# Kernel optimization log

Hardware: AMD Instinct MI355X
Metric: run time of the kernel (lower is better)

Reference implementation:

```python
import jax, jax.numpy as jnp
import numpy as np

B, N, D, H = 8, 8192, 512, 8  # batch, seq, hidden, heads
DH = D // H


def _rope_tables(n, d, dtype=jnp.float32):
    # standard rotate-half RoPE tables over the full hidden dim (d/2 freq pairs)
    half = d // 2
    inv_freq = 1.0 / (10000.0 ** (np.arange(0, half, dtype=np.float32) / half))
    pos = np.arange(n, dtype=np.float32)
    ang = np.einsum('n,f->nf', pos, inv_freq)          # [N, D/2]
    ang = np.concatenate([ang, ang], axis=-1)          # [N, D]
    return jnp.asarray(np.cos(ang), dtype), jnp.asarray(np.sin(ang), dtype)


def setup_inputs() -> dict:
    key = jax.random.key(0)
    k1, k2 = jax.random.split(key)
    hidden_states = jax.random.normal(k1, (B, N, D), dtype=jnp.float32)
    num_layers = 24
    std = 0.02 / np.sqrt(2.0 * num_layers * D)
    W = jax.random.normal(k2, (D, D), dtype=jnp.float32) * std
    cos, sin = _rope_tables(N, D)
    return {"hidden_states": hidden_states, "W": W, "cos": cos, "sin": sin}


def _rotate_half(x):
    x1, x2 = jnp.split(x, 2, axis=-1)
    return jnp.concatenate([-x2, x1], axis=-1)


def reference(hidden_states, W, cos, sin):
    # dropout(p=0) in eval mode -> identity
    x = hidden_states * cos + _rotate_half(hidden_states) * sin  # RoPE, [B,N,D]
    q = jnp.einsum('bnd,ed->bne', x, W)                          # F.linear(x, W)
    qh = q.reshape(B, N, H, DH)
    xh = x.reshape(B, N, H, DH)
    # linear-complexity path: (K^T V) then Q @ (.), per head
    kv = jnp.einsum('bnhd,bnhe->bhde', xh, xh)   # [B,H,DH,DH]
    out = jnp.einsum('bnhd,bhde->bnhe', qh, kv)  # [B,N,H,DH]
    return out.reshape(B, N, D)
```

## Files before the change

### kernel.cpp

```cpp
#include <hip/hip_runtime.h>
#include <hip/hip_bf16.h>
#include <stdint.h>

#define BB 8
#define NN 8192
#define DD 512
#define HH 8
#define DHD 64
#define NCH 32

typedef __attribute__((ext_vector_type(8))) short bf16x8;
typedef __attribute__((ext_vector_type(4))) float f32x4;
typedef __attribute__((ext_vector_type(4))) float f4v;

__device__ __forceinline__ unsigned short f2bf(float f) {
  union { float f; unsigned int u; } v; v.f = f;
  return (unsigned short)((v.u + 0x7FFFu + ((v.u >> 16) & 1u)) >> 16);
}

__device__ __forceinline__ unsigned cvtpk(float lo, float hi) {
  unsigned r;
  asm("v_cvt_pk_bf16_f32 %0, %1, %2" : "=v"(r) : "v"(lo), "v"(hi));
  return r;
}

__device__ __forceinline__ void async16(const void* g, void* l) {
  __builtin_amdgcn_global_load_lds(
      (const __attribute__((address_space(1))) void*)g,
      (__attribute__((address_space(3))) void*)l, 16, 0, 0);
}

__global__ __launch_bounds__(1024, 4) void ropekv_kernel(
    const float* __restrict__ h, const float* __restrict__ cs,
    const float* __restrict__ sn, unsigned short* __restrict__ x,
    float* __restrict__ kvp, int nbh) {
  __shared__ __align__(16) unsigned int xt32[2][512 * 34];
  int blk = blockIdx.x;
  int chunk = blk & 31, b = blk >> 5;
  int tid = threadIdx.x;
  int wave = tid >> 6, lane = tid & 63;
  int rpar = lane & 1;
  int g = lane >> 1;
  int cf = g * 8;
  int l15 = lane & 15, q = lane >> 4;
  int head = wave >> 1;
  int half = wave & 1;
  int hd = head * 64;
  size_t row0 = (size_t)b * NN + (size_t)chunk * 256;
  int n0 = chunk * 256;

  f32x4 acc[2][4];
#pragma unroll
  for (int i = 0; i < 2; ++i)
#pragma unroll
    for (int j = 0; j < 4; ++j) acc[i][j] = (f32x4){0.f, 0.f, 0.f, 0.f};

  f4v ha[2][2], hb[2][2];

  auto loadt = [&](int t) {
#pragma unroll
    for (int p = 0; p < 2; ++p) {
      int r = 2 * (wave + 16 * p) + rpar;
      const float* hp = h + (row0 + t * 64 + r) * DD + cf;
      ha[p][0] = __builtin_nontemporal_load((const f4v*)hp);
      ha[p][1] = __builtin_nontemporal_load((const f4v*)(hp + 4));
      hb[p][0] = __builtin_nontemporal_load((const f4v*)(hp + 256));
      hb[p][1] = __builtin_nontemporal_load((const f4v*)(hp + 260));
    }
  };

  auto ropet = [&](int t) {
    int pb = t & 1;
#pragma unroll
    for (int p = 0; p < 2; ++p) {
      int r = 2 * (wave + 16 * p) + rpar;
      int nr = n0 + t * 64 + r;
      const float* cp = cs + (size_t)nr * DD + cf;
      const float* sp = sn + (size_t)nr * DD + cf;
      f4v c0 = *(const f4v*)cp, c1 = *(const f4v*)(cp + 4);
      f4v s0 = *(const f4v*)sp, s1 = *(const f4v*)(sp + 4);
      f4v xl0 = ha[p][0] * c0 - hb[p][0] * s0;
      f4v xl1 = ha[p][1] * c1 - hb[p][1] * s1;
      f4v xh0 = hb[p][0] * c0 + ha[p][0] * s0;
      f4v xh1 = hb[p][1] * c1 + ha[p][1] * s1;
      unsigned ml[4], mh[4];
      ml[0] = cvtpk(xl0.x, xl0.y);
      ml[1] = cvtpk(xl0.z, xl0.w);
      ml[2] = cvtpk(xl1.x, xl1.y);
      ml[3] = cvtpk(xl1.z, xl1.w);
      mh[0] = cvtpk(xh0.x, xh0.y);
      mh[1] = cvtpk(xh0.z, xh0.w);
      mh[2] = cvtpk(xh1.x, xh1.y);
      mh[3] = cvtpk(xh1.z, xh1.w);
      unsigned short* xp = x + (row0 + t * 64 + r) * DD + cf;
      uint4 st0; st0.x = ml[0]; st0.y = ml[1]; st0.z = ml[2]; st0.w = ml[3];
      uint4 st1; st1.x = mh[0]; st1.y = mh[1]; st1.z = mh[2]; st1.w = mh[3];
      *(uint4*)xp         = st0;
      *(uint4*)(xp + 256) = st1;
      unsigned pk[8];
#pragma unroll
      for (int k = 0; k < 4; ++k) {
        unsigned mine = rpar ? mh[k] : ml[k];
        unsigned send = rpar ? ml[k] : mh[k];
        unsigned recv = (unsigned)__shfl_xor((int)send, 1, 64);
        if (!rpar) {
          pk[2 * k]     = (mine & 0xffffu) | (recv << 16);
          pk[2 * k + 1] = (mine >> 16) | (recv & 0xffff0000u);
        } else {
          pk[2 * k]     = (recv & 0xffffu) | (mine << 16);
          pk[2 * k + 1] = (recv >> 16) | (mine & 0xffff0000u);
        }
      }
      int np = wave + 16 * p;
      int dbase = cf + (rpar ? 256 : 0);
      int rot = (g >> 1) & 7;
#pragma unroll
      for (int w = 0; w < 8; ++w) {
        int jj = (w + rot) & 7;
        xt32[pb][(dbase + jj) * 34 + np] = pk[jj];
      }
    }
  };

  auto mfmat = [&](int t) {
    const unsigned short* xt16 = (const unsigned short*)xt32[t & 1];
#pragma unroll
    for (int ks = 0; ks < 64; ks += 32) {
      bf16x8 af[2], bf[4];
#pragma unroll
      for (int i = 0; i < 2; ++i)
        af[i] = *(const bf16x8*)&xt16[(hd + half * 32 + i * 16 + l15) * 68 + ks + q * 8];
#pragma unroll
      for (int j = 0; j < 4; ++j)
        bf[j] = *(const bf16x8*)&xt16[(hd + j * 16 + l15) * 68 + ks + q * 8];
#pragma unroll
      for (int i = 0; i < 2; ++i)
#pragma unroll
        for (int j = 0; j < 4; ++j)
          acc[i][j] = __builtin_amdgcn_mfma_f32_16x16x32_bf16(af[i], bf[j], acc[i][j], 0, 0, 0);
    }
  };

  loadt(0);
  ropet(0);
  loadt(1);
  __syncthreads();
#pragma unroll
  for (int t = 0; t < 4; ++t) {
    if (t < 3) ropet(t + 1);
    if (t < 2) loadt(t + 2);
    mfmat(t);
    __syncthreads();
  }

  int bh = b * 8 + head;
  float* dst = kvp + ((size_t)chunk * nbh + bh) * 4096;
#pragma unroll
  for (int i = 0; i < 2; ++i)
#pragma unroll
    for (int j = 0; j < 4; ++j)
#pragma unroll
      for (int reg = 0; reg < 4; ++reg)
        dst[(half * 32 + i * 16 + q * 4 + reg) * 64 + j * 16 + l15] = acc[i][j][reg];
}

__global__ __launch_bounds__(512, 2) void wkvt_kernel(
    const float* __restrict__ W, const float* __restrict__ kvp,
    unsigned short* __restrict__ wkvt, int nbh) {
  __shared__ float kvs[64 * 16];
  __shared__ __align__(16) float ws[64 * 512];
  int blk = blockIdx.x;
  int bh = blk >> 2, eq = blk & 3;
  int b = bh >> 3, hh = bh & 7;
  int tid = threadIdx.x;
  if (tid < 256) {
    int idx = tid * 4;
    int d = idx >> 4, ec = idx & 15;
    f4v s = (f4v){0.f, 0.f, 0.f, 0.f};
    for (int c = 0; c < NCH; ++c)
      s += *(const f4v*)&kvp[((size_t)c * nbh + bh) * 4096 + d * 64 + eq * 16 + ec];
    *(f4v*)&kvs[idx] = s;
  }
#pragma unroll
  for (int i = 0; i < 16; ++i) {
    int idx = i * 2048 + tid * 4;
    *(f4v*)&ws[idx] = *(const f4v*)&W[(size_t)(hh * DHD + (idx >> 9)) * DD + (idx & 511)];
  }
  __syncthreads();
  int el = tid & 15, fg = tid >> 4;
  f4v av[4];
#pragma unroll
  for (int k = 0; k < 4; ++k) av[k] = (f4v){0.f, 0.f, 0.f, 0.f};
#pragma unroll 8
  for (int d = 0; d < 64; ++d) {
    float kvv = kvs[d * 16 + el];
    const f4v* wr = (const f4v*)&ws[d * DD + fg * 16];
#pragma unroll
    for (int k = 0; k < 4; ++k) av[k] += wr[k] * kvv;
  }
  unsigned short tb[16];
#pragma unroll
  for (int k = 0; k < 4; ++k) {
    tb[k * 4 + 0] = f2bf(av[k].x); tb[k * 4 + 1] = f2bf(av[k].y);
    tb[k * 4 + 2] = f2bf(av[k].z); tb[k * 4 + 3] = f2bf(av[k].w);
  }
  size_t ob = ((size_t)b * DD + hh * DHD + eq * 16 + el) * DD + fg * 16;
  *(uint4*)&wkvt[ob]     = *(uint4*)&tb[0];
  *(uint4*)&wkvt[ob + 8] = *(uint4*)&tb[8];
}

__global__ __launch_bounds__(256, 3) void gemm_kernel(const unsigned short* __restrict__ x,
                                                      const unsigned short* __restrict__ wkvt,
                                                      float* __restrict__ out) {
  __shared__ __align__(16) unsigned short As[128 * 64];
  __shared__ __align__(16) unsigned short Bs[128 * 64];
  int mt = blockIdx.x, ct = blockIdx.y, bz = blockIdx.z;
  int tid = threadIdx.x, wave = tid >> 6, lane = tid & 63;
  int wm = wave & 1, wn = wave >> 1;
  int l15 = lane & 15, q = lane >> 4;
  int lrow = lane >> 3, lcol = (lane & 7) * 8;
  const unsigned short* Ag = x    + ((size_t)bz * NN + mt * 128) * DD;
  const unsigned short* Bg = wkvt + ((size_t)bz * DD + ct * 128) * DD;
  f32x4 acc[4][4];
#pragma unroll
  for (int i = 0; i < 4; ++i)
#pragma unroll
    for (int j = 0; j < 4; ++j) acc[i][j] = (f32x4){0.f, 0.f, 0.f, 0.f};

  for (int kk = 0; kk < 512; kk += 64) {
#pragma unroll
    for (int i = 0; i < 4; ++i)
      async16(Ag + (size_t)(wave * 32 + i * 8 + lrow) * DD + kk + lcol,
              &As[(wave * 32 + i * 8) * 64]);
#pragma unroll
    for (int i = 0; i < 4; ++i)
      async16(Bg + (size_t)(wave * 32 + i * 8 + lrow) * DD + kk + lcol,
              &Bs[(wave * 32 + i * 8) * 64]);
    __syncthreads();
#pragma unroll
    for (int ks = 0; ks < 64; ks += 32) {
      bf16x8 a[4], bb[4];
#pragma unroll
      for (int i = 0; i < 4; ++i)
        a[i] = *(const bf16x8*)&As[(wm * 64 + i * 16 + l15) * 64 + ks + q * 8];
#pragma unroll
      for (int j = 0; j < 4; ++j)
        bb[j] = *(const bf16x8*)&Bs[(wn * 64 + j * 16 + l15) * 64 + ks + q * 8];
#pragma unroll
      for (int i = 0; i < 4; ++i)
#pragma unroll
        for (int j = 0; j < 4; ++j)
          acc[i][j] = __builtin_amdgcn_mfma_f32_16x16x32_bf16(a[i], bb[j], acc[i][j], 0, 0, 0);
    }
    __syncthreads();
  }
  float* ob = out + ((size_t)bz * NN + mt * 128 + wm * 64) * DD + ct * 128 + wn * 64;
#pragma unroll
  for (int i = 0; i < 4; ++i)
#pragma unroll
    for (int j = 0; j < 4; ++j) {
      int row = i * 16 + q * 4;
      int col = j * 16 + l15;
#pragma unroll
      for (int reg = 0; reg < 4; ++reg)
        __builtin_nontemporal_store(acc[i][j][reg], &ob[(size_t)(row + reg) * DD + col]);
    }
}

extern "C" void kernel_launch(void* const* d_in, const int* in_sizes, int n_in,
                              void* d_out, int out_size, void* d_ws, size_t ws_size,
                              hipStream_t stream) {
  (void)in_sizes; (void)n_in; (void)out_size;
  const float* h  = (const float*)d_in[0];
  const float* W  = (const float*)d_in[1];
  const float* cs = (const float*)d_in[2];
  const float* sn = (const float*)d_in[3];
  float* out = (float*)d_out;

  const size_t x_full     = (size_t)BB * NN * DD * 2;
  const size_t kvp_full   = (size_t)NCH * BB * HH * DHD * DHD * 4;
  const size_t wkvt_full  = (size_t)BB * DD * DD * 2;
  const size_t x_batch    = (size_t)NN * DD * 2;
  const size_t kvp_batch  = (size_t)NCH * HH * DHD * DHD * 4;
  const size_t wkvt_batch = (size_t)DD * DD * 2;

  if (ws_size >= x_full + kvp_full + wkvt_full) {
    unsigned short* xw   = (unsigned short*)d_ws;
    float*          kvp  = (float*)((char*)d_ws + x_full);
    unsigned short* wkvt = (unsigned short*)((char*)d_ws + x_full + kvp_full);
    ropekv_kernel<<<dim3(BB * 32), dim3(1024), 0, stream>>>(h, cs, sn, xw, kvp, BB * HH);
    wkvt_kernel<<<dim3(BB * HH * 4), dim3(512), 0, stream>>>(W, kvp, wkvt, BB * HH);
    gemm_kernel<<<dim3(NN / 128, DD / 128, BB), dim3(256), 0, stream>>>(xw, wkvt, out);
  } else {
    unsigned short* xw   = (unsigned short*)d_ws;
    float*          kvp  = (float*)((char*)d_ws + x_batch);
    unsigned short* wkvt = (unsigned short*)((char*)d_ws + x_batch + kvp_batch);
    for (int b = 0; b < BB; ++b) {
      ropekv_kernel<<<dim3(32), dim3(1024), 0, stream>>>(
          h + (size_t)b * NN * DD, cs, sn, xw, kvp, HH);
      wkvt_kernel<<<dim3(HH * 4), dim3(512), 0, stream>>>(W, kvp, wkvt, HH);
      gemm_kernel<<<dim3(NN / 128, DD / 128, 1), dim3(256), 0, stream>>>(
          xw, wkvt, out + (size_t)b * NN * DD);
    }
  }
}
```

Before: 322.1 us.

## Switch GEMM to 32x32x16 MFMA with XOR-swizzled LDS tiles

Rewrites the main GEMM inner loop to use 32x32x16 bf16 MFMA instructions in a 2x2 accumulator grid instead of the 4x4 grid of 16x16x32. The LDS tiles are loaded with an XOR swizzle on the 16-byte chunk index to avoid bank conflicts on the fragment reads. Launch bounds are raised to 4 blocks per CU. The larger MFMA needs fewer LDS fragment reads per FLOP. The risks are register pressure under the tighter occupancy bound and a strided output store pattern.

```diff
diff --git a/kernel.cpp b/kernel.cpp
--- a/kernel.cpp
+++ b/kernel.cpp
@@ -11,6 +11,7 @@
 
 typedef __attribute__((ext_vector_type(8))) short bf16x8;
 typedef __attribute__((ext_vector_type(4))) float f32x4;
+typedef __attribute__((ext_vector_type(16))) float f32x16;
 typedef __attribute__((ext_vector_type(4))) float f4v;
 
 __device__ __forceinline__ unsigned short f2bf(float f) {
@@ -209,7 +210,7 @@
   *(uint4*)&wkvt[ob + 8] = *(uint4*)&tb[8];
 }
 
-__global__ __launch_bounds__(256, 3) void gemm_kernel(const unsigned short* __restrict__ x,
+__global__ __launch_bounds__(256, 4) void gemm_kernel(const unsigned short* __restrict__ x,
                                                       const unsigned short* __restrict__ wkvt,
                                                       float* __restrict__ out) {
   __shared__ __align__(16) unsigned short As[128 * 64];
@@ -217,54 +218,68 @@
   int mt = blockIdx.x, ct = blockIdx.y, bz = blockIdx.z;
   int tid = threadIdx.x, wave = tid >> 6, lane = tid & 63;
   int wm = wave & 1, wn = wave >> 1;
-  int l15 = lane & 15, q = lane >> 4;
-  int lrow = lane >> 3, lcol = (lane & 7) * 8;
+  int l31 = lane & 31, hk = lane >> 5;
   const unsigned short* Ag = x    + ((size_t)bz * NN + mt * 128) * DD;
   const unsigned short* Bg = wkvt + ((size_t)bz * DD + ct * 128) * DD;
-  f32x4 acc[4][4];
-#pragma unroll
-  for (int i = 0; i < 4; ++i)
-#pragma unroll
-    for (int j = 0; j < 4; ++j) acc[i][j] = (f32x4){0.f, 0.f, 0.f, 0.f};
+
+  int su_row[4], su_ss[4];
+#pragma unroll
+  for (int i = 0; i < 4; ++i) {
+    int u = i * 256 + tid;
+    su_row[i] = u >> 3;
+    su_ss[i]  = (u & 7) ^ ((u >> 3) & 7);
+  }
+
+  f32x16 acc[2][2];
+#pragma unroll
+  for (int mi = 0; mi < 2; ++mi)
+#pragma unroll
+    for (int ni = 0; ni < 2; ++ni)
+#pragma unroll
+      for (int r = 0; r < 16; ++r) acc[mi][ni][r] = 0.f;
 
   for (int kk = 0; kk < 512; kk += 64) {
 #pragma unroll
-    for (int i = 0; i < 4; ++i)
-      async16(Ag + (size_t)(wave * 32 + i * 8 + lrow) * DD + kk + lcol,
-              &As[(wave * 32 + i * 8) * 64]);
-#pragma unroll
-    for (int i = 0; i < 4; ++i)
-      async16(Bg + (size_t)(wave * 32 + i * 8 + lrow) * DD + kk + lcol,
-              &Bs[(wave * 32 + i * 8) * 64]);
+    for (int i = 0; i < 4; ++i) {
+      int u = i * 256 + tid;
+      async16(Ag + (size_t)su_row[i] * DD + kk + su_ss[i] * 8, &As[u * 8]);
+      async16(Bg + (size_t)su_row[i] * DD + kk + su_ss[i] * 8, &Bs[u * 8]);
+    }
     __syncthreads();
 #pragma unroll
-    for (int ks = 0; ks < 64; ks += 32) {
-      bf16x8 a[4], bb[4];
-#pragma unroll
-      for (int i = 0; i < 4; ++i)
-        a[i] = *(const bf16x8*)&As[(wm * 64 + i * 16 + l15) * 64 + ks + q * 8];
-#pragma unroll
-      for (int j = 0; j < 4; ++j)
-        bb[j] = *(const bf16x8*)&Bs[(wn * 64 + j * 16 + l15) * 64 + ks + q * 8];
-#pragma unroll
-      for (int i = 0; i < 4; ++i)
-#pragma unroll
-        for (int j = 0; j < 4; ++j)
-          acc[i][j] = __builtin_amdgcn_mfma_f32_16x16x32_bf16(a[i], bb[j], acc[i][j], 0, 0, 0);
+    for (int ks = 0; ks < 64; ks += 16) {
+      bf16x8 a[2], bb[2];
+#pragma unroll
+      for (int mi = 0; mi < 2; ++mi) {
+        int row = wm * 64 + mi * 32 + l31;
+        int s = ((ks >> 3) + hk) ^ (row & 7);
+        a[mi] = *(const bf16x8*)&As[row * 64 + s * 8];
+      }
+#pragma unroll
+      for (int ni = 0; ni < 2; ++ni) {
+        int row = wn * 64 + ni * 32 + l31;
+        int s = ((ks >> 3) + hk) ^ (row & 7);
+        bb[ni] = *(const bf16x8*)&Bs[row * 64 + s * 8];
+      }
+#pragma unroll
+      for (int mi = 0; mi < 2; ++mi)
+#pragma unroll
+        for (int ni = 0; ni < 2; ++ni)
+          acc[mi][ni] = __builtin_amdgcn_mfma_f32_32x32x16_bf16(a[mi], bb[ni], acc[mi][ni], 0, 0, 0);
     }
     __syncthreads();
   }
-  float* ob = out + ((size_t)bz * NN + mt * 128 + wm * 64) * DD + ct * 128 + wn * 64;
-#pragma unroll
-  for (int i = 0; i < 4; ++i)
-#pragma unroll
-    for (int j = 0; j < 4; ++j) {
-      int row = i * 16 + q * 4;
-      int col = j * 16 + l15;
-#pragma unroll
-      for (int reg = 0; reg < 4; ++reg)
-        __builtin_nontemporal_store(acc[i][j][reg], &ob[(size_t)(row + reg) * DD + col]);
-    }
+  float* ob = out + ((size_t)bz * NN + mt * 128) * DD + ct * 128;
+#pragma unroll
+  for (int mi = 0; mi < 2; ++mi)
+#pragma unroll
+    for (int ni = 0; ni < 2; ++ni)
+#pragma unroll
+      for (int r = 0; r < 16; ++r) {
+        int row = wm * 64 + mi * 32 + (r & 3) + 8 * (r >> 2) + 4 * hk;
+        int col = wn * 64 + ni * 32 + l31;
+        __builtin_nontemporal_store(acc[mi][ni][r], &ob[(size_t)row * DD + col]);
+      }
 }
 
 extern "C" void kernel_launch(void* const* d_in, const int* in_sizes, int n_in,
```

After: 310.7 us. -3.5%, faster.
